# Performance work log

Measured on AMD Instinct MI355X. Metric: run time of the kernel, lower is better.

The kernel has to match this reference:

```python
import jax, jax.numpy as jnp
import numpy as np

B, T, HID = 1, 1024, 2048
H, DK, DV, M, KW = 16, 128, 128, 128, 4  # heads, key dim, value dim, slots, conv kernel
SCALE = DK ** -0.5
EPS = 1e-5


def short_conv(x, w):
    # causal depthwise conv1d + silu; x: [B,T,C], w: [C,K]
    K = w.shape[1]
    xp = jnp.pad(x, ((0, 0), (K - 1, 0), (0, 0)))
    t = x.shape[1]
    y = sum(xp[:, i:i + t] * w[:, i] for i in range(K))
    return jax.nn.silu(y)


def l2norm(x):
    return x * jax.lax.rsqrt(jnp.sum(x * x, axis=-1, keepdims=True) + 1e-6)


def gsa2_scan(q, k, v, w, g, beta):
    # q,k: [B,T,H,DK]  v: [B,T,H,DV]  w,g: [B,T,H,M]  beta: [B,T,H]
    b = q.shape[0]
    tm = lambda x: jnp.moveaxis(x, 1, 0)  # time-major
    Sk0 = jnp.zeros((b, H, DK, M), q.dtype)  # key->slot memory
    Sv0 = jnp.zeros((b, H, M, DV), q.dtype)  # slot->value memory

    def step(carry, xs):
        Sk, Sv = carry
        q_t, k_t, v_t, w_t, g_t, b_t = xs
        gt = jnp.exp(g_t)  # [B,H,M] gate in (0,1) since g = logsigmoid(.)
        bw = b_t[:, :, None] * w_t  # beta-scaled slot write address [B,H,M]
        Sk = Sk * gt[:, :, None, :] + k_t[..., :, None] * bw[:, :, None, :]
        Sv = Sv * gt[..., None] + bw[..., None] * v_t[:, :, None, :]
        s = jnp.einsum('bhd,bhdm->bhm', q_t, Sk) * SCALE
        a = jax.nn.softmax(s, axis=-1)
        o_t = jnp.einsum('bhm,bhmd->bhd', a, Sv)
        return (Sk, Sv), o_t

    (_, _), o = jax.lax.scan(step, (Sk0, Sv0),
                             (tm(q), tm(k), tm(v), tm(w), tm(g), tm(beta)))
    return jnp.moveaxis(o, 0, 1)  # [B,T,H,DV]


def reference(hidden_states, Wq, Wk, Wv, Ww, cq, ck, cv,
              Wf1, Wf2, Wb, Wg1, Wg2, bg2, norm_w, Wo):
    h = hidden_states  # [B,T,HID]
    q = short_conv(h @ Wq, cq)
    k = short_conv(h @ Wk, ck)
    v = short_conv(h @ Wv, cv)
    w = short_conv(h @ Ww, cv)  # source applies v_conv1d to w (faithful)
    g = jax.nn.log_sigmoid((h @ Wf1) @ Wf2)   # [B,T,H*M]
    beta = jax.nn.sigmoid(h @ Wb)             # [B,T,H]
    rs = lambda x, d: x.reshape(x.shape[0], x.shape[1], -1, d)
    q, k = rs(q, DK), rs(k, DK)
    v = rs(v, DV)
    w = l2norm(rs(w, M))
    g = rs(g, M)
    o = gsa2_scan(q, k, v, w, g, beta)        # [B,T,H,DV]
    gate = rs((h @ Wg1) @ Wg2 + bg2, DV)
    # FusedRMSNormGated with sigmoid activation
    o = o * jax.lax.rsqrt(jnp.mean(o * o, axis=-1, keepdims=True) + EPS)
    o = o * norm_w * jax.nn.sigmoid(gate)
    o = o.reshape(o.shape[0], o.shape[1], -1)
    return o @ Wo


def setup_inputs() -> dict:
    key = jax.random.key(0)
    ks = jax.random.split(key, 16)
    s = 0.02
    return {
        'hidden_states': jax.random.normal(ks[0], (B, T, HID), jnp.float32),
        'Wq': jax.random.normal(ks[1], (HID, H * DK), jnp.float32) * s,
        'Wk': jax.random.normal(ks[2], (HID, H * DK), jnp.float32) * s,
        'Wv': jax.random.normal(ks[3], (HID, H * DV), jnp.float32) * s,
        'Ww': jax.random.normal(ks[4], (HID, H * M), jnp.float32) * s,
        'cq': jax.random.normal(ks[5], (H * DK, KW), jnp.float32) * 0.2,
        'ck': jax.random.normal(ks[6], (H * DK, KW), jnp.float32) * 0.2,
        'cv': jax.random.normal(ks[7], (H * DV, KW), jnp.float32) * 0.2,
        'Wf1': jax.random.normal(ks[8], (HID, DV), jnp.float32) * s,
        'Wf2': jax.random.normal(ks[9], (DV, H * M), jnp.float32) * s,
        'Wb': jax.random.normal(ks[10], (HID, H), jnp.float32) * s,
        'Wg1': jax.random.normal(ks[11], (HID, DV), jnp.float32) * s,
        'Wg2': jax.random.normal(ks[12], (DV, H * DV), jnp.float32) * s,
        'bg2': jnp.zeros((H * DV,), jnp.float32),
        'norm_w': jnp.ones((DV,), jnp.float32),
        'Wo': jax.random.normal(ks[13], (H * DV, HID), jnp.float32) * s,
    }
```

## Files before the change

### kernel.cpp

```cpp
#include <hip/hip_runtime.h>
#include <hip/hip_bf16.h>
#include <stdint.h>

typedef unsigned short u16;
typedef __attribute__((ext_vector_type(8))) short bf16x8;
typedef __attribute__((ext_vector_type(4))) short bf16x4;
typedef __attribute__((ext_vector_type(4))) float f32x4;

#define DEV static __device__ __forceinline__

DEV u16 f2bf(float f){
  union { float f; unsigned u; } x; x.f = f;
  unsigned r = x.u + 0x7fffu + ((x.u >> 16) & 1u);
  return (u16)(r >> 16);
}

DEV float bf2f(u16 u){
  union { unsigned u; float f; } x; x.u = ((unsigned)u) << 16; return x.f;
}

DEV bf16x8 ldfrag(const u16* p){
  bf16x4 a = *(const bf16x4*)p;
  bf16x4 b = *(const bf16x4*)(p+4);
  bf16x8 r;
  r[0]=a[0]; r[1]=a[1]; r[2]=a[2]; r[3]=a[3];
  r[4]=b[0]; r[5]=b[1]; r[6]=b[2]; r[7]=b[3];
  return r;
}

DEV bf16x4 cvt4(float a, float b, float c, float d){
  bf16x4 r; r[0]=(short)f2bf(a); r[1]=(short)f2bf(b); r[2]=(short)f2bf(c); r[3]=(short)f2bf(d);
  return r;
}

DEV void g2l16(const void* g, void* l){
  __builtin_amdgcn_global_load_lds((const __attribute__((address_space(1))) unsigned int*)g,
                                   (__attribute__((address_space(3))) unsigned int*)l,
                                   16, 0, 0);
}

__global__ __launch_bounds__(256)
void transp64_k(const float* __restrict__ Wq, const float* __restrict__ Wk,
                const float* __restrict__ Wv, const float* __restrict__ Ww,
                const float* __restrict__ Wo, u16* __restrict__ WcatT, u16* __restrict__ WoT,
                const float* __restrict__ hX, u16* __restrict__ h_bf,
                const float* __restrict__ Wf1, const float* __restrict__ Wg1,
                const float* __restrict__ Wf2, const float* __restrict__ Wg2,
                u16* __restrict__ WfgT, u16* __restrict__ Wf2T, u16* __restrict__ Wg2T){
  __shared__ float tile[64*65];
  const int z = blockIdx.z;
  if (z == 5){
    int idx = ((blockIdx.y*32 + blockIdx.x)*256 + threadIdx.x)*8;
    float4 v0 = *(const float4*)&hX[idx];
    float4 v1 = *(const float4*)&hX[idx+4];
    ushort4 o0, o1;
    o0.x=f2bf(v0.x); o0.y=f2bf(v0.y); o0.z=f2bf(v0.z); o0.w=f2bf(v0.w);
    o1.x=f2bf(v1.x); o1.y=f2bf(v1.y); o1.z=f2bf(v1.z); o1.w=f2bf(v1.w);
    *(ushort4*)&h_bf[idx]   = o0;
    *(ushort4*)&h_bf[idx+4] = o1;
    return;
  }
  if (z >= 6){
    int rem = blockIdx.y*32 + blockIdx.x;
    if (rem >= 256) return;
    const float* src; u16* dst; int R, C, cx, cy;
    if (z==6){      src=Wf1; dst=WfgT;                  R=2048; C=128;  cx=rem&3;  cy=rem>>2; }
    else if (z==7){ src=Wg1; dst=WfgT+(size_t)128*2048; R=2048; C=128;  cx=rem&3;  cy=rem>>2; }
    else if (z==8){ src=Wf2; dst=Wf2T;                  R=128;  C=2048; cx=rem>>2; cy=rem&3; }
    else {          src=Wg2; dst=Wg2T;                  R=128;  C=2048; cx=rem>>2; cy=rem&3; }
    const int c0 = cx*32, r0 = cy*32;
    const int x = threadIdx.x & 31, y0 = threadIdx.x >> 5;
#pragma unroll
    for (int j=0;j<4;j++){
      int r = y0 + j*8;
      tile[r*33 + x] = src[(size_t)(r0+r)*C + c0 + x];
    }
    __syncthreads();
#pragma unroll
    for (int j=0;j<4;j++){
      int cc = y0 + j*8;
      dst[(size_t)(c0+cc)*R + r0 + x] = f2bf(tile[x*33 + cc]);
    }
    return;
  }
  const float* src = (z==0)?Wq:((z==1)?Wk:((z==2)?Wv:((z==3)?Ww:Wo)));
  u16* dst = (z<4) ? (WcatT + (size_t)z*4194304) : WoT;
  const int c0 = blockIdx.x*64, r0 = blockIdx.y*64;
#pragma unroll
  for (int p=0;p<4;p++){
    int i = threadIdx.x + p*256;
    int r = i>>4, c4 = (i&15)<<2;
    *(float4*)&tile[r*65 + c4] = *(const float4*)&src[(size_t)(r0+r)*2048 + c0 + c4];
  }
  __syncthreads();
#pragma unroll
  for (int p=0;p<4;p++){
    int i = threadIdx.x + p*256;
    int cc = i>>4, r4 = (i&15)<<2;
    ushort4 o;
    o.x = f2bf(tile[(r4+0)*65 + cc]); o.y = f2bf(tile[(r4+1)*65 + cc]);
    o.z = f2bf(tile[(r4+2)*65 + cc]); o.w = f2bf(tile[(r4+3)*65 + cc]);
    *(ushort4*)&dst[(size_t)(c0+cc)*2048 + r0 + r4] = o;
  }
}

template<bool OBF>
__global__ __launch_bounds__(256)
void gemm4_k(const u16* __restrict__ A, const u16* __restrict__ B, void* __restrict__ Cp,
             int K, int lda, int ldb, int ldc){
  __shared__ u16 As[2][128*64];
  __shared__ u16 Bs[2][128*64];
  const int m0 = blockIdx.y*128, n0 = blockIdx.x*128;
  const int tid = threadIdx.x;
  const int wave = tid>>6, lane = tid&63, lr = lane&15, kg = lane>>4;
  const int wm = wave>>1, wn = wave&1;
  const f32x4 vz = {0.f,0.f,0.f,0.f};
  f32x4 acc[4][4];
#pragma unroll
  for (int a=0;a<4;a++)
#pragma unroll
    for (int b=0;b<4;b++) acc[a][b]=vz;

#define STAGE4(buf, k0) do { \
    _Pragma("unroll") \
    for (int p=0;p<4;p++){ \
      int chunk = tid + p*256, r_ = chunk>>3, ci = chunk&7; \
      g2l16(A + (size_t)(m0+r_)*lda + (k0) + ((ci^(r_&7))<<3), &As[buf][chunk*8]); \
    } \
    _Pragma("unroll") \
    for (int p=0;p<4;p++){ \
      int chunk = tid + p*256, r_ = chunk>>3, ci = chunk&7; \
      g2l16(B + (size_t)(n0+r_)*ldb + (k0) + ((ci^(r_&7))<<3), &Bs[buf][chunk*8]); \
    } \
  } while(0)

  const int nt = K>>6;
  STAGE4(0, 0);
  STAGE4(1, 64);
  for (int t=0; t<nt; ++t){
    const int buf = t&1;
    if (t < nt-1) asm volatile("s_waitcnt vmcnt(8)" ::: "memory");
    else          asm volatile("s_waitcnt vmcnt(0)" ::: "memory");
    asm volatile("s_barrier" ::: "memory");
#pragma unroll
    for (int ks=0; ks<2; ++ks){
      bf16x8 af[4], bfv[4];
#pragma unroll
      for (int mi=0;mi<4;mi++){
        int r = wm*64+mi*16+lr;
        af[mi] = *(const bf16x8*)&As[buf][r*64 + (((ks*4+kg)^(r&7))<<3)];
      }
#pragma unroll
      for (int ni=0;ni<4;ni++){
        int r = wn*64+ni*16+lr;
        bfv[ni] = *(const bf16x8*)&Bs[buf][r*64 + (((ks*4+kg)^(r&7))<<3)];
      }
      asm volatile("s_waitcnt lgkmcnt(0)" ::: "memory");
      __builtin_amdgcn_sched_barrier(0);
      __builtin_amdgcn_s_setprio(1);
#pragma unroll
      for (int mi=0;mi<4;mi++)
#pragma unroll
        for (int ni=0;ni<4;ni++)
          acc[mi][ni] = __builtin_amdgcn_mfma_f32_16x16x32_bf16(af[mi], bfv[ni], acc[mi][ni], 0, 0, 0);
      __builtin_amdgcn_s_setprio(0);
      __builtin_amdgcn_sched_barrier(0);
      asm volatile("s_barrier" ::: "memory");
    }
    if (t+2 < nt) STAGE4(buf, (t+2)<<6);
  }
#undef STAGE4
#pragma unroll
  for (int mi=0;mi<4;mi++)
#pragma unroll
    for (int ni=0;ni<4;ni++)
#pragma unroll
      for (int vv=0;vv<4;vv++){
        int row = m0 + wm*64 + mi*16 + kg*4 + vv;
        int col = n0 + wn*64 + ni*16 + lr;
        if (OBF) ((u16*)Cp)[(size_t)row*ldc + col] = f2bf(acc[mi][ni][vv]);
        else     ((float*)Cp)[(size_t)row*ldc + col] = acc[mi][ni][vv];
      }
}

__global__ __launch_bounds__(256)
void gemm4sk_k(const u16* __restrict__ A, const u16* __restrict__ B, float* __restrict__ P,
               int Khalf, int lda, int ldb, int ldc){
  __shared__ u16 As[2][128*64];
  __shared__ u16 Bs[2][128*64];
  const int m0 = blockIdx.y*128, n0 = blockIdx.x*128;
  const int kbase = blockIdx.z*Khalf;
  const int tid = threadIdx.x;
  const int wave = tid>>6, lane = tid&63, lr = lane&15, kg = lane>>4;
  const int wm = wave>>1, wn = wave&1;
  const f32x4 vz = {0.f,0.f,0.f,0.f};
  f32x4 acc[4][4];
#pragma unroll
  for (int a=0;a<4;a++)
#pragma unroll
    for (int b=0;b<4;b++) acc[a][b]=vz;

#define STAGE4(buf, k0) do { \
    _Pragma("unroll") \
    for (int p=0;p<4;p++){ \
      int chunk = tid + p*256, r_ = chunk>>3, ci = chunk&7; \
      g2l16(A + (size_t)(m0+r_)*lda + (k0) + ((ci^(r_&7))<<3), &As[buf][chunk*8]); \
    } \
    _Pragma("unroll") \
    for (int p=0;p<4;p++){ \
      int chunk = tid + p*256, r_ = chunk>>3, ci = chunk&7; \
      g2l16(B + (size_t)(n0+r_)*ldb + (k0) + ((ci^(r_&7))<<3), &Bs[buf][chunk*8]); \
    } \
  } while(0)

  const int nt = Khalf>>6;
  STAGE4(0, kbase);
  STAGE4(1, kbase+64);
  for (int t=0; t<nt; ++t){
    const int buf = t&1;
    if (t < nt-1) asm volatile("s_waitcnt vmcnt(8)" ::: "memory");
    else          asm volatile("s_waitcnt vmcnt(0)" ::: "memory");
    asm volatile("s_barrier" ::: "memory");
#pragma unroll
    for (int ks=0; ks<2; ++ks){
      bf16x8 af[4], bfv[4];
#pragma unroll
      for (int mi=0;mi<4;mi++){
        int r = wm*64+mi*16+lr;
        af[mi] = *(const bf16x8*)&As[buf][r*64 + (((ks*4+kg)^(r&7))<<3)];
      }
#pragma unroll
      for (int ni=0;ni<4;ni++){
        int r = wn*64+ni*16+lr;
        bfv[ni] = *(const bf16x8*)&Bs[buf][r*64 + (((ks*4+kg)^(r&7))<<3)];
      }
      asm volatile("s_waitcnt lgkmcnt(0)" ::: "memory");
      __builtin_amdgcn_sched_barrier(0);
      __builtin_amdgcn_s_setprio(1);
#pragma unroll
      for (int mi=0;mi<4;mi++)
#pragma unroll
        for (int ni=0;ni<4;ni++)
          acc[mi][ni] = __builtin_amdgcn_mfma_f32_16x16x32_bf16(af[mi], bfv[ni], acc[mi][ni], 0, 0, 0);
      __builtin_amdgcn_s_setprio(0);
      __builtin_amdgcn_sched_barrier(0);
      asm volatile("s_barrier" ::: "memory");
    }
    if (t+2 < nt) STAGE4(buf, kbase + ((t+2)<<6));
  }
#undef STAGE4
#pragma unroll
  for (int mi=0;mi<4;mi++)
#pragma unroll
    for (int ni=0;ni<4;ni++)
#pragma unroll
      for (int vv=0;vv<4;vv++){
        int row = m0 + wm*64 + mi*16 + kg*4 + vv;
        int col = n0 + wn*64 + ni*16 + lr;
        P[(size_t)blockIdx.z*2097152 + (size_t)row*ldc + col] = acc[mi][ni][vv];
      }
}

__global__ __launch_bounds__(256)
void addout_k(const float* __restrict__ P, float* __restrict__ out){
  int i = (blockIdx.x*256 + threadIdx.x)*4;
  float4 a = *(const float4*)&P[i];
  float4 b = *(const float4*)&P[2097152 + i];
  float4 s = {a.x+b.x, a.y+b.y, a.z+b.z, a.w+b.w};
  *(float4*)&out[i] = s;
}

__global__ __launch_bounds__(256)
void gemmg_k(const u16* __restrict__ f1g1, const u16* __restrict__ Bf, const u16* __restrict__ Bg,
             float* __restrict__ Cf, float* __restrict__ Cg){
  __shared__ u16 As[128*32];
  __shared__ u16 Bs[128*32];
  const int zz = blockIdx.z;
  const u16* A = f1g1 + zz*128;
  const u16* B = zz ? Bg : Bf;
  float* C = zz ? Cg : Cf;
  const int m0 = blockIdx.y*128, n0 = blockIdx.x*128;
  const int tid = threadIdx.x;
  const int lane = tid & 63, wave = tid >> 6;
  const int wr = wave >> 1, wc = wave & 1;
  const int lr = lane & 15, kg = lane >> 4;
  const f32x4 vzero = {0.f,0.f,0.f,0.f};
  f32x4 acc[4][4];
#pragma unroll
  for (int a=0;a<4;a++)
#pragma unroll
    for (int b=0;b<4;b++) acc[a][b] = vzero;
  const int r0 = tid>>2, s0 = tid&3;
  for (int k0=0;k0<128;k0+=32){
    __syncthreads();
    g2l16(A + (size_t)(m0+r0)*256 + k0 + s0*8, (u16*)As + (size_t)tid*8);
    g2l16(B + (size_t)(n0+r0)*128 + k0 + s0*8, (u16*)Bs + (size_t)tid*8);
    g2l16(A + (size_t)(m0+r0+64)*256 + k0 + s0*8, (u16*)As + (size_t)(tid+256)*8);
    g2l16(B + (size_t)(n0+r0+64)*128 + k0 + s0*8, (u16*)Bs + (size_t)(tid+256)*8);
    __syncthreads();
    bf16x8 af[4], bfv[4];
#pragma unroll
    for (int mi=0;mi<4;mi++) af[mi]  = *(const bf16x8*)(As + (wr*64+mi*16+lr)*32 + kg*8);
#pragma unroll
    for (int ni=0;ni<4;ni++) bfv[ni] = *(const bf16x8*)(Bs + (wc*64+ni*16+lr)*32 + kg*8);
#pragma unroll
    for (int mi=0;mi<4;mi++)
#pragma unroll
      for (int ni=0;ni<4;ni++)
        acc[mi][ni] = __builtin_amdgcn_mfma_f32_16x16x32_bf16(af[mi], bfv[ni], acc[mi][ni], 0, 0, 0);
  }
#pragma unroll
  for (int mi=0;mi<4;mi++)
#pragma unroll
    for (int ni=0;ni<4;ni++)
#pragma unroll
      for (int vv=0;vv<4;vv++){
        int row = m0 + wr*64 + mi*16 + kg*4 + vv;
        int col = n0 + wc*64 + ni*16 + lr;
        float val = acc[mi][ni][vv];
        if (zz==0) val = fminf(val,0.f) - __logf(1.f + __expf(-fabsf(val)));
        C[(size_t)row*2048 + col] = val;
      }
}

__global__ __launch_bounds__(256)
void gemmsk_k(const u16* __restrict__ A, const u16* __restrict__ B, float* __restrict__ P,
              int lda, int ldb){
  __shared__ u16 As[128*32];
  __shared__ u16 Bs[128*32];
  const int m0 = blockIdx.y*128, n0 = blockIdx.x*128;
  const int kbase = blockIdx.z*128;
  const int tid = threadIdx.x;
  const int lane = tid & 63, wave = tid >> 6;
  const int wr = wave >> 1, wc = wave & 1;
  const int lr = lane & 15, kg = lane >> 4;
  const f32x4 vzero = {0.f,0.f,0.f,0.f};
  f32x4 acc[4][4];
#pragma unroll
  for (int a=0;a<4;a++)
#pragma unroll
    for (int b=0;b<4;b++) acc[a][b] = vzero;
  const int r0 = tid>>2, s0 = tid&3;
  for (int k0=kbase;k0<kbase+128;k0+=32){
    __syncthreads();
    g2l16(A + (size_t)(m0+r0)*lda + k0 + s0*8, (u16*)As + (size_t)tid*8);
    g2l16(B + (size_t)(n0+r0)*ldb + k0 + s0*8, (u16*)Bs + (size_t)tid*8);
    g2l16(A + (size_t)(m0+r0+64)*lda + k0 + s0*8, (u16*)As + (size_t)(tid+256)*8);
    g2l16(B + (size_t)(n0+r0+64)*ldb + k0 + s0*8, (u16*)Bs + (size_t)(tid+256)*8);
    __syncthreads();
    bf16x8 af[4], bfv[4];
#pragma unroll
    for (int mi=0;mi<4;mi++) af[mi]  = *(const bf16x8*)(As + (wr*64+mi*16+lr)*32 + kg*8);
#pragma unroll
    for (int ni=0;ni<4;ni++) bfv[ni] = *(const bf16x8*)(Bs + (wc*64+ni*16+lr)*32 + kg*8);
#pragma unroll
    for (int mi=0;mi<4;mi++)
#pragma unroll
      for (int ni=0;ni<4;ni++)
        acc[mi][ni] = __builtin_amdgcn_mfma_f32_16x16x32_bf16(af[mi], bfv[ni], acc[mi][ni], 0, 0, 0);
  }
#pragma unroll
  for (int mi=0;mi<4;mi++)
#pragma unroll
    for (int ni=0;ni<4;ni++)
#pragma unroll
      for (int vv=0;vv<4;vv++){
        int row = m0 + wr*64 + mi*16 + kg*4 + vv;
        int col = n0 + wc*64 + ni*16 + lr;
        P[(size_t)blockIdx.z*262144 + (size_t)row*256 + col] = acc[mi][ni][vv];
      }
}

__global__ __launch_bounds__(256)
void reduce16_k(const float* __restrict__ P, u16* __restrict__ out){
  int i = (blockIdx.x*256 + threadIdx.x)*4;
  float4 s = *(const float4*)&P[i];
#pragma unroll
  for (int z=1;z<16;z++){
    float4 p = *(const float4*)&P[(size_t)z*262144 + i];
    s.x+=p.x; s.y+=p.y; s.z+=p.z; s.w+=p.w;
  }
  ushort4 o; o.x=f2bf(s.x); o.y=f2bf(s.y); o.z=f2bf(s.z); o.w=f2bf(s.w);
  *(ushort4*)&out[i] = o;
}

__global__ __launch_bounds__(256)
void beta_k(const float* __restrict__ h, const float* __restrict__ Wb, float* __restrict__ betab){
  __shared__ float hrow[2048];
  __shared__ float red[16][5];
  const int t = blockIdx.x, tid = threadIdx.x;
#pragma unroll
  for (int j=0;j<8;j++) hrow[tid + j*256] = h[(size_t)t*2048 + tid + j*256];
  __syncthreads();
  float part[16];
#pragma unroll
  for (int n=0;n<16;n++) part[n]=0.f;
  for (int j=0;j<8;j++){
    int kk = tid + j*256;
    float hv = hrow[kk];
    const float4* wr4 = (const float4*)&Wb[(size_t)kk*16];
    float4 w0=wr4[0], w1=wr4[1], w2=wr4[2], w3=wr4[3];
    part[0]+=hv*w0.x; part[1]+=hv*w0.y; part[2]+=hv*w0.z; part[3]+=hv*w0.w;
    part[4]+=hv*w1.x; part[5]+=hv*w1.y; part[6]+=hv*w1.z; part[7]+=hv*w1.w;
    part[8]+=hv*w2.x; part[9]+=hv*w2.y; part[10]+=hv*w2.z; part[11]+=hv*w2.w;
    part[12]+=hv*w3.x; part[13]+=hv*w3.y; part[14]+=hv*w3.z; part[15]+=hv*w3.w;
  }
#pragma unroll
  for (int n=0;n<16;n++){
    float s = part[n];
#pragma unroll
    for (int off=1;off<64;off<<=1) s += __shfl_xor(s, off);
    if ((tid&63)==0) red[n][tid>>6] = s;
  }
  __syncthreads();
  if (tid < 16){
    float s = red[tid][0]+red[tid][1]+red[tid][2]+red[tid][3];
    betab[t*16+tid] = 1.f/(1.f+__expf(-s));
  }
}

__global__ __launch_bounds__(256)
void conv_k(const u16* __restrict__ raw, const float* __restrict__ cq,
            const float* __restrict__ ck, const float* __restrict__ cv,
            const float* __restrict__ betab,
            u16* __restrict__ qo, u16* __restrict__ ko,
            u16* __restrict__ vo, float* __restrict__ bwout){
  __shared__ float red[2][2][4];
  int idx = blockIdx.x*256 + threadIdx.x;
  int cgl = idx & 8191, tb = idx >> 13;
  int which = cgl >> 11, cc = cgl & 2047;
  const float* wt = (which==0)?cq:((which==1)?ck:cv);
  float4 w4 = *(const float4*)&wt[cc*4];
  int t0 = tb*4;
  float x[7];
#pragma unroll
  for (int j=0;j<7;j++){
    int t = t0 - 3 + j;
    x[j] = (t >= 0) ? bf2f(raw[(size_t)t*8192 + cgl]) : 0.f;
  }
  float y[4];
#pragma unroll
  for (int j=0;j<4;j++){
    float yy = x[j]*w4.x + x[j+1]*w4.y + x[j+2]*w4.z + x[j+3]*w4.w;
    y[j] = yy / (1.f + __expf(-yy));
  }
  if (which < 3){
    u16* outb = (which==0)?qo:((which==1)?ko:vo);
#pragma unroll
    for (int j=0;j<4;j++)
      outb[(size_t)(t0+j)*2048 + cc] = f2bf(y[j]);
  } else {
    const int hh = threadIdx.x >> 7;
    const int wh = (threadIdx.x >> 6) & 1;
    float ss[4];
#pragma unroll
    for (int j=0;j<4;j++){
      float s = y[j]*y[j];
#pragma unroll
      for (int off=1;off<64;off<<=1) s += __shfl_xor(s, off);
      ss[j] = s;
    }
    if ((threadIdx.x & 63) == 0){
#pragma unroll
      for (int j=0;j<4;j++) red[hh][wh][j] = ss[j];
    }
    __syncthreads();
    const int h = cc >> 7;
#pragma unroll
    for (int j=0;j<4;j++){
      float tot = red[hh][0][j] + red[hh][1][j];
      float r = rsqrtf(tot + 1e-6f) * betab[(t0+j)*16 + h];
      bwout[(size_t)(t0+j)*2048 + cc] = y[j]*r;
    }
  }
}

__global__ __launch_bounds__(128)
void cg_k(const float* __restrict__ gpre, float* __restrict__ cg){
  int idx = blockIdx.x*128 + threadIdx.x;
  int c = idx >> 11;
  size_t base = (size_t)(idx & 2047);
  float run = 0.f;
  for (int i2=0;i2<64;i2++){
    size_t t = (size_t)c*64 + i2;
    run += gpre[t*2048 + base];
    cg[t*2048 + base] = run;
  }
}

__global__ __launch_bounds__(256)
void phaseA_k(const u16* __restrict__ k, const u16* __restrict__ v,
              const float* __restrict__ bw, const float* __restrict__ cg,
              u16* __restrict__ DSkT, u16* __restrict__ DSvT){
  __shared__ u16 UT[128*68];
  __shared__ u16 KT[128*68];
  __shared__ u16 VT[128*68];
  __shared__ float Gt[128];
  const int bx=blockIdx.x, h=bx&15, c=bx>>4, tid=threadIdx.x;
  const int w=tid>>6, lane=tid&63, lr=lane&15, kg=lane>>4;
  if (tid<128) Gt[tid] = cg[(size_t)(c*64+63)*2048 + h*128 + tid];
  __syncthreads();
#pragma unroll
  for (int j=0;j<8;j++){
    int f4=tid+j*256, r=f4>>5, c4=(f4&31)<<2;
    size_t g=(size_t)(c*64+r)*2048 + h*128 + c4;
    ushort4 kv=*(const ushort4*)&k[g];
    ushort4 vv=*(const ushort4*)&v[g];
    float4 bv=*(const float4*)&bw[g];
    float4 cv=*(const float4*)&cg[g];
    float u0=bv.x*__expf(Gt[c4+0]-cv.x);
    float u1=bv.y*__expf(Gt[c4+1]-cv.y);
    float u2=bv.z*__expf(Gt[c4+2]-cv.z);
    float u3=bv.w*__expf(Gt[c4+3]-cv.w);
    KT[(c4+0)*68+r]=kv.x; KT[(c4+1)*68+r]=kv.y;
    KT[(c4+2)*68+r]=kv.z; KT[(c4+3)*68+r]=kv.w;
    VT[(c4+0)*68+r]=vv.x; VT[(c4+1)*68+r]=vv.y;
    VT[(c4+2)*68+r]=vv.z; VT[(c4+3)*68+r]=vv.w;
    UT[(c4+0)*68+r]=f2bf(u0);   UT[(c4+1)*68+r]=f2bf(u1);
    UT[(c4+2)*68+r]=f2bf(u2);   UT[(c4+3)*68+r]=f2bf(u3);
  }
  __syncthreads();
  const f32x4 vz = {0.f,0.f,0.f,0.f};
  {
    f32x4 acc[2][8];
#pragma unroll
    for (int a=0;a<2;a++)
#pragma unroll
      for (int b=0;b<8;b++) acc[a][b]=vz;
#pragma unroll
    for (int ks=0;ks<2;ks++){
      bf16x8 a0=ldfrag(&UT[(w*32   +lr)*68 + ks*32+kg*8]);
      bf16x8 a1=ldfrag(&UT[(w*32+16+lr)*68 + ks*32+kg*8]);
#pragma unroll
      for (int nj=0;nj<8;nj++){
        bf16x8 b=ldfrag(&KT[(nj*16+lr)*68 + ks*32+kg*8]);
        acc[0][nj]=__builtin_amdgcn_mfma_f32_16x16x32_bf16(a0,b,acc[0][nj],0,0,0);
        acc[1][nj]=__builtin_amdgcn_mfma_f32_16x16x32_bf16(a1,b,acc[1][nj],0,0,0);
      }
    }
#pragma unroll
    for (int mi2=0;mi2<2;mi2++)
#pragma unroll
      for (int nj=0;nj<8;nj++)
#pragma unroll
        for (int vv2=0;vv2<4;vv2++)
          DSkT[(size_t)bx*16384 + (size_t)(w*32+mi2*16+kg*4+vv2)*128 + nj*16+lr] = f2bf(acc[mi2][nj][vv2]);
  }
  {
    f32x4 acc[2][8];
#pragma unroll
    for (int a=0;a<2;a++)
#pragma unroll
      for (int b=0;b<8;b++) acc[a][b]=vz;
#pragma unroll
    for (int ks=0;ks<2;ks++){
      bf16x8 a0=ldfrag(&VT[(w*32   +lr)*68 + ks*32+kg*8]);
      bf16x8 a1=ldfrag(&VT[(w*32+16+lr)*68 + ks*32+kg*8]);
#pragma unroll
      for (int nj=0;nj<8;nj++){
        bf16x8 b=ldfrag(&UT[(nj*16+lr)*68 + ks*32+kg*8]);
        acc[0][nj]=__builtin_amdgcn_mfma_f32_16x16x32_bf16(a0,b,acc[0][nj],0,0,0);
        acc[1][nj]=__builtin_amdgcn_mfma_f32_16x16x32_bf16(a1,b,acc[1][nj],0,0,0);
      }
    }
#pragma unroll
    for (int mi2=0;mi2<2;mi2++)
#pragma unroll
      for (int nj=0;nj<8;nj++)
#pragma unroll
        for (int vv2=0;vv2<4;vv2++)
          DSvT[(size_t)bx*16384 + (size_t)(w*32+mi2*16+kg*4+vv2)*128 + nj*16+lr] = f2bf(acc[mi2][nj][vv2]);
  }
}

__global__ __launch_bounds__(256)
void phaseB_k(const u16* __restrict__ DSk, const u16* __restrict__ DSv,
              const float* __restrict__ cg, u16* __restrict__ Sk0, u16* __restrict__ Sv0){
  unsigned idx = blockIdx.x*256u + threadIdx.x;
  int sel  = idx >> 18;
  int h    = (idx >> 14) & 15;
  int flat = idx & 16383;
  int mdec = sel ? (flat & 127) : (flat >> 7);
  const u16* DS = sel ? DSv : DSk;
  u16* S = sel ? Sv0 : Sk0;
  float cur = 0.f;
  for (int c=0;c<16;c++){
    size_t sb = ((size_t)(c*16+h))*16384 + flat;
    S[sb] = f2bf(cur);
    float gd = __expf(cg[(size_t)(c*64+63)*2048 + h*128 + mdec]);
    cur = cur*gd + bf2f(DS[sb]);
  }
}

__global__ __launch_bounds__(256)
void phaseC_k(const u16* __restrict__ q, const u16* __restrict__ k,
              const u16* __restrict__ v, const float* __restrict__ bw,
              const float* __restrict__ cg, const u16* __restrict__ SkT,
              const u16* __restrict__ SvT, float* __restrict__ o){
  __shared__ u16 Qb[64*132];
  __shared__ u16 KV[8704];
  __shared__ u16 Bws[64*132];
  __shared__ u16 BwT[128*68];
  __shared__ u16 Ssb[64*68];
  __shared__ u16 SkL[128*132];
  __shared__ u16 SvL[128*132];
  __shared__ float cgm[128];
  __shared__ float ecgm[128];
  const int bx=blockIdx.x, h=bx&15, c=bx>>4, tid=threadIdx.x;
  const int w=tid>>6, lane=tid&63, lr=lane&15, kg=lane>>4;
  const float SCALE = 0.088388347648318447f;
  const f32x4 vz = {0.f,0.f,0.f,0.f};
  if (tid<128){ float t=cg[(size_t)(c*64+31)*2048 + h*128 + tid]; cgm[tid]=t; ecgm[tid]=__expf(t); }
  __syncthreads();
#pragma unroll
  for (int j=0;j<8;j++){
    int f4=tid+j*256, r=f4>>5, c4=(f4&31)<<2;
    size_t g=(size_t)(c*64+r)*2048 + h*128 + c4;
    *(ushort4*)&Qb[r*132+c4] = *(const ushort4*)&q[g];
    *(ushort4*)&KV[r*132+c4] = *(const ushort4*)&k[g];
    float4 bv=*(const float4*)&bw[g];
    float4 cv=*(const float4*)&cg[g];
    float b0=bv.x*__expf(cgm[c4+0]-cv.x);
    float b1=bv.y*__expf(cgm[c4+1]-cv.y);
    float b2=bv.z*__expf(cgm[c4+2]-cv.z);
    float b3=bv.w*__expf(cgm[c4+3]-cv.w);
    bf16x4 bb = cvt4(b0,b1,b2,b3);
    *(bf16x4*)&Bws[r*132+c4] = bb;
    BwT[(c4+0)*68+r]=(u16)bb[0]; BwT[(c4+1)*68+r]=(u16)bb[1];
    BwT[(c4+2)*68+r]=(u16)bb[2]; BwT[(c4+3)*68+r]=(u16)bb[3];
  }
  __syncthreads();
  {
    f32x4 acc1[4];
#pragma unroll
    for (int a=0;a<4;a++) acc1[a]=vz;
#pragma unroll
    for (int ks=0;ks<4;ks++){
      bf16x8 aq = ldfrag(&Qb[(w*16+lr)*132 + ks*32+kg*8]);
#pragma unroll
      for (int ni=0;ni<4;ni++){
        bf16x8 bk = ldfrag(&KV[(ni*16+lr)*132 + ks*32+kg*8]);
        acc1[ni]=__builtin_amdgcn_mfma_f32_16x16x32_bf16(aq,bk,acc1[ni],0,0,0);
      }
    }
#pragma unroll
    for (int ni=0;ni<4;ni++)
#pragma unroll
      for (int vv2=0;vv2<4;vv2++){
        int row=w*16+kg*4+vv2, col=ni*16+lr;
        Ssb[row*68+col] = (col<=row) ? f2bf(acc1[ni][vv2]) : (u16)0;
      }
  }
  __syncthreads();
#pragma unroll
  for (int j=0;j<8;j++){
    int f4=tid+j*256, r=f4>>5, c4=(f4&31)<<2;
    ushort4 vv=*(const ushort4*)&v[(size_t)(c*64+r)*2048 + h*128 + c4];
    KV[(c4+0)*68+r]=vv.x; KV[(c4+1)*68+r]=vv.y;
    KV[(c4+2)*68+r]=vv.z; KV[(c4+3)*68+r]=vv.w;
  }
#pragma unroll
  for (int j=0;j<16;j++){
    int f4=tid+j*256, r=f4>>5, c4=(f4&31)<<2;
    ushort4 s4=*(const ushort4*)&SkT[(size_t)bx*16384 + (size_t)r*128 + c4];
    float em=ecgm[r];
    *(bf16x4*)&SkL[r*132+c4]=cvt4(bf2f(s4.x)*em, bf2f(s4.y)*em, bf2f(s4.z)*em, bf2f(s4.w)*em);
  }
#pragma unroll
  for (int j=0;j<16;j++){
    int f4=tid+j*256, r=f4>>5, c4=(f4&31)<<2;
    ushort4 s4=*(const ushort4*)&SvT[(size_t)bx*16384 + (size_t)r*128 + c4];
    *(bf16x4*)&SvL[r*132+c4]=cvt4(bf2f(s4.x)*ecgm[c4+0], bf2f(s4.y)*ecgm[c4+1],
                                  bf2f(s4.z)*ecgm[c4+2], bf2f(s4.w)*ecgm[c4+3]);
  }
  f32x4 zac[8];
#pragma unroll
  for (int a=0;a<8;a++) zac[a]=vz;
#pragma unroll
  for (int ks=0;ks<2;ks++){
    bf16x8 as_ = ldfrag(&Ssb[(w*16+lr)*68 + ks*32+kg*8]);
#pragma unroll
    for (int ni=0;ni<8;ni++){
      bf16x8 bb = ldfrag(&BwT[(ni*16+lr)*68 + ks*32+kg*8]);
      zac[ni]=__builtin_amdgcn_mfma_f32_16x16x32_bf16(as_,bb,zac[ni],0,0,0);
    }
  }
  __syncthreads();
#pragma unroll
  for (int dt=0;dt<4;dt++){
    bf16x8 aq = ldfrag(&Qb[(w*16+lr)*132 + dt*32+kg*8]);
#pragma unroll
    for (int ni=0;ni<8;ni++){
      bf16x8 bs = ldfrag(&SkL[(ni*16+lr)*132 + dt*32+kg*8]);
      zac[ni]=__builtin_amdgcn_mfma_f32_16x16x32_bf16(aq,bs,zac[ni],0,0,0);
    }
  }
  float dec[4][8], zz[4][8];
#pragma unroll
  for (int vv2=0;vv2<4;vv2++)
#pragma unroll
    for (int ni=0;ni<8;ni++) zz[vv2][ni]=zac[ni][vv2];
#pragma unroll
  for (int vv2=0;vv2<4;vv2++){
    size_t gr=(size_t)(c*64+w*16+kg*4+vv2)*2048 + h*128;
#pragma unroll
    for (int ni=0;ni<8;ni++){
      float cgv = cg[gr + ni*16+lr];
      dec[vv2][ni] = __expf(cgv - cgm[ni*16+lr]);
    }
  }
#pragma unroll
  for (int vv2=0;vv2<4;vv2++){
    float mx=-3.0e38f;
#pragma unroll
    for (int ni=0;ni<8;ni++){ zz[vv2][ni] *= SCALE*dec[vv2][ni]; mx=fmaxf(mx,zz[vv2][ni]); }
    mx=fmaxf(mx,__shfl_xor(mx,1)); mx=fmaxf(mx,__shfl_xor(mx,2));
    mx=fmaxf(mx,__shfl_xor(mx,4)); mx=fmaxf(mx,__shfl_xor(mx,8));
    float sum=0.f;
#pragma unroll
    for (int ni=0;ni<8;ni++){ zz[vv2][ni]=__expf(zz[vv2][ni]-mx); sum+=zz[vv2][ni]; }
    sum+=__shfl_xor(sum,1); sum+=__shfl_xor(sum,2);
    sum+=__shfl_xor(sum,4); sum+=__shfl_xor(sum,8);
    float inv=1.f/sum;
#pragma unroll
    for (int ni=0;ni<8;ni++) zz[vv2][ni] *= inv*dec[vv2][ni];
  }
#pragma unroll
  for (int vv2=0;vv2<4;vv2++)
#pragma unroll
    for (int ni=0;ni<8;ni++)
      Qb[(w*16+kg*4+vv2)*132 + ni*16+lr] = f2bf(zz[vv2][ni]);
  {
    f32x4 acc4[4];
#pragma unroll
    for (int a=0;a<4;a++) acc4[a]=vz;
#pragma unroll
    for (int ks=0;ks<4;ks++){
      bf16x8 aa = ldfrag(&Qb[(w*16+lr)*132 + ks*32+kg*8]);
#pragma unroll
      for (int ni=0;ni<4;ni++){
        bf16x8 bb = ldfrag(&Bws[(ni*16+lr)*132 + ks*32+kg*8]);
        acc4[ni]=__builtin_amdgcn_mfma_f32_16x16x32_bf16(aa,bb,acc4[ni],0,0,0);
      }
    }
#pragma unroll
    for (int ni=0;ni<4;ni++)
#pragma unroll
      for (int vv2=0;vv2<4;vv2++){
        int row=w*16+kg*4+vv2, col=ni*16+lr;
        Ssb[row*68+col] = (col<=row) ? f2bf(acc4[ni][vv2]) : (u16)0;
      }
  }
  f32x4 oac[8];
#pragma unroll
  for (int a=0;a<8;a++) oac[a]=vz;
#pragma unroll
  for (int ks=0;ks<2;ks++){
    bf16x8 ap = ldfrag(&Ssb[(w*16+lr)*68 + ks*32+kg*8]);
#pragma unroll
    for (int ni=0;ni<8;ni++){
      bf16x8 bv2 = ldfrag(&KV[(ni*16+lr)*68 + ks*32+kg*8]);
      oac[ni]=__builtin_amdgcn_mfma_f32_16x16x32_bf16(ap,bv2,oac[ni],0,0,0);
    }
  }
#pragma unroll
  for (int mt=0;mt<4;mt++){
    bf16x8 aa = ldfrag(&Qb[(w*16+lr)*132 + mt*32+kg*8]);
#pragma unroll
    for (int ni=0;ni<8;ni++){
      bf16x8 bs = ldfrag(&SvL[(ni*16+lr)*132 + mt*32+kg*8]);
      oac[ni]=__builtin_amdgcn_mfma_f32_16x16x32_bf16(aa,bs,oac[ni],0,0,0);
    }
  }
#pragma unroll
  for (int ni=0;ni<8;ni++)
#pragma unroll
    for (int vv2=0;vv2<4;vv2++)
      o[(size_t)(c*64+w*16+kg*4+vv2)*2048 + h*128 + ni*16+lr] = oac[ni][vv2];
}

__global__ __launch_bounds__(256)
void norm_k(const float* __restrict__ o, const float* __restrict__ gate,
            const float* __restrict__ bg2, const float* __restrict__ nw,
            u16* __restrict__ Obf){
  int row = blockIdx.x*4 + (threadIdx.x>>6);
  int lane = threadIdx.x & 63;
  int t = row >> 4, h = row & 15;
  size_t base = (size_t)t*2048 + h*128;
  float o0 = o[base+lane], o1 = o[base+64+lane];
  float ss = o0*o0 + o1*o1;
#pragma unroll
  for (int off=1;off<64;off<<=1) ss += __shfl_xor(ss, off);
  float r = rsqrtf(ss*(1.f/128.f) + 1e-5f);
  int hv0 = h*128+lane, hv1 = hv0+64;
  float g0 = gate[base+lane]    + bg2[hv0];
  float g1 = gate[base+64+lane] + bg2[hv1];
  float v0 = o0*r*nw[lane]   *(1.f/(1.f+__expf(-g0)));
  float v1 = o1*r*nw[lane+64]*(1.f/(1.f+__expf(-g1)));
  Obf[base+lane]    = f2bf(v0);
  Obf[base+64+lane] = f2bf(v1);
}

extern "C" void kernel_launch(void* const* d_in, const int* in_sizes, int n_in,
                              void* d_out, int out_size, void* d_ws, size_t ws_size,
                              hipStream_t stream){
  (void)in_sizes; (void)n_in; (void)out_size; (void)ws_size;
  const float* hX   = (const float*)d_in[0];
  const float* Wq   = (const float*)d_in[1];
  const float* Wk   = (const float*)d_in[2];
  const float* Wv   = (const float*)d_in[3];
  const float* Ww   = (const float*)d_in[4];
  const float* cq   = (const float*)d_in[5];
  const float* ck   = (const float*)d_in[6];
  const float* cv   = (const float*)d_in[7];
  const float* Wf1  = (const float*)d_in[8];
  const float* Wf2  = (const float*)d_in[9];
  const float* Wb   = (const float*)d_in[10];
  const float* Wg1  = (const float*)d_in[11];
  const float* Wg2  = (const float*)d_in[12];
  const float* bg2  = (const float*)d_in[13];
  const float* nw   = (const float*)d_in[14];
  const float* Wo   = (const float*)d_in[15];
  char* ws = (char*)d_ws;
  u16*   h_bf  = (u16*)  (ws + 0);
  u16*   WcatT = (u16*)  (ws + 4194304);
  u16*   Sk0   = (u16*)  (ws + 4194304);
  u16*   Sv0   = (u16*)  (ws + 20971520);
  u16*   WoT   = (u16*)  (ws + 37748736);
  u16*   WfgT  = (u16*)  (ws + 46137344);
  u16*   Wf2T  = (u16*)  (ws + 47185920);
  u16*   Wg2T  = (u16*)  (ws + 47710208);
  u16*   qkvw  = (u16*)  (ws + 48234496);
  u16*   DSk   = (u16*)  (ws + 48234496);
  u16*   DSv   = (u16*)  (ws + 56623104);
  float* Pw    = (float*)(ws + 48234496);
  float* gateb = (float*)(ws + 65011712);
  u16*   qb    = (u16*)  (ws + 81788928);
  u16*   kb    = (u16*)  (ws + 90177536);
  u16*   vb    = (u16*)  (ws + 98566144);
  float* P8    = (float*)(ws + 106954752);
  float* osc   = (float*)(ws + 106954752);
  float* bwb   = (float*)(ws + 115343360);
  u16*   f1g1  = (u16*)  (ws + 123731968);
  float* gpre  = (float*)(ws + 124256256);
  float* cgb   = (float*)(ws + 132644864);
  float* betab = (float*)(ws + 141033472);
  u16*   Obf   = (u16*)  (ws + 141099008);
  float* outp  = (float*)d_out;

  transp64_k<<<dim3(32,32,10),256,0,stream>>>(Wq, Wk, Wv, Ww, Wo, WcatT, WoT, hX, h_bf,
                                              Wf1, Wg1, Wf2, Wg2, WfgT, Wf2T, Wg2T);

  gemm4_k<true><<<dim3(64,8),256,0,stream>>>(h_bf, WcatT, qkvw, 2048, 2048, 2048, 8192);
  gemmsk_k<<<dim3(2,8,16),256,0,stream>>>(h_bf, WfgT, P8, 2048, 2048);
  reduce16_k<<<256,256,0,stream>>>(P8, f1g1);
  gemmg_k<<<dim3(16,8,2),256,0,stream>>>(f1g1, Wf2T, Wg2T, gpre, gateb);
  beta_k<<<1024,256,0,stream>>>(hX, Wb, betab);

  conv_k<<<8192,256,0,stream>>>(qkvw, cq, ck, cv, betab, qb, kb, vb, bwb);
  cg_k<<<256,128,0,stream>>>(gpre, cgb);

  phaseA_k<<<256,256,0,stream>>>(kb, vb, bwb, cgb, DSk, DSv);
  phaseB_k<<<2048,256,0,stream>>>(DSk, DSv, cgb, Sk0, Sv0);
  phaseC_k<<<256,256,0,stream>>>(qb, kb, vb, bwb, cgb, Sk0, Sv0, osc);

  norm_k<<<4096,256,0,stream>>>(osc, gateb, bg2, nw, Obf);
  gemm4sk_k<<<dim3(16,8,2),256,0,stream>>>(Obf, WoT, Pw, 1024, 2048, 2048, 2048);
  addout_k<<<2048,256,0,stream>>>(Pw, outp);
}
```

Measured before the change: 191.8 us.

## Fuse gate cumsum into gemm epilogue and RMSNorm-gating into phaseC

The chunk-local cumulative sum of log-sigmoid gates moves into the gemmg_k epilogue, which uses in-register prefix sums plus wave shuffles across each 64-row tile, so cg_k disappears. The output RMSNorm with sigmoid gating is fused into phaseC_k's epilogue, removing norm_k and the fp32 output round trip. The gate projection is stored as bf16, and beta_k reads the bf16 copy of the hidden states. Together these cut two launches and several fp32 global-memory passes, at the cost of bf16 precision on the gate and on beta's input.

```diff
diff --git a/kernel.cpp b/kernel.cpp
--- a/kernel.cpp
+++ b/kernel.cpp
@@ -272,13 +272,12 @@
 
 __global__ __launch_bounds__(256)
 void gemmg_k(const u16* __restrict__ f1g1, const u16* __restrict__ Bf, const u16* __restrict__ Bg,
-             float* __restrict__ Cf, float* __restrict__ Cg){
+             float* __restrict__ Ccg, u16* __restrict__ Cgate){
   __shared__ u16 As[128*32];
   __shared__ u16 Bs[128*32];
   const int zz = blockIdx.z;
   const u16* A = f1g1 + zz*128;
   const u16* B = zz ? Bg : Bf;
-  float* C = zz ? Cg : Cf;
   const int m0 = blockIdx.y*128, n0 = blockIdx.x*128;
   const int tid = threadIdx.x;
   const int lane = tid & 63, wave = tid >> 6;
@@ -309,18 +308,56 @@
       for (int ni=0;ni<4;ni++)
         acc[mi][ni] = __builtin_amdgcn_mfma_f32_16x16x32_bf16(af[mi], bfv[ni], acc[mi][ni], 0, 0, 0);
   }
-#pragma unroll
-  for (int mi=0;mi<4;mi++)
-#pragma unroll
-    for (int ni=0;ni<4;ni++)
-#pragma unroll
-      for (int vv=0;vv<4;vv++){
-        int row = m0 + wr*64 + mi*16 + kg*4 + vv;
-        int col = n0 + wc*64 + ni*16 + lr;
-        float val = acc[mi][ni][vv];
-        if (zz==0) val = fminf(val,0.f) - __logf(1.f + __expf(-fabsf(val)));
-        C[(size_t)row*2048 + col] = val;
-      }
+  if (zz == 0){
+#pragma unroll
+    for (int ni=0;ni<4;ni++){
+      float p[4][4]; float s[4];
+#pragma unroll
+      for (int mi=0;mi<4;mi++){
+        float run = 0.f;
+#pragma unroll
+        for (int vv=0;vv<4;vv++){
+          float v = acc[mi][ni][vv];
+          v = fminf(v,0.f) - __logf(1.f + __expf(-fabsf(v)));
+          run += v; p[mi][vv] = run;
+        }
+        s[mi] = run;
+      }
+      float M = 0.f; float base[4];
+#pragma unroll
+      for (int mi=0;mi<4;mi++){
+        float a0 = __shfl(s[mi], lr);
+        float a1 = __shfl(s[mi], lr+16);
+        float a2 = __shfl(s[mi], lr+32);
+        float a3 = __shfl(s[mi], lr+48);
+        float before = 0.f;
+        if (kg>0) before += a0;
+        if (kg>1) before += a1;
+        if (kg>2) before += a2;
+        base[mi] = M + before;
+        M += a0+a1+a2+a3;
+      }
+#pragma unroll
+      for (int mi=0;mi<4;mi++)
+#pragma unroll
+        for (int vv=0;vv<4;vv++){
+          int row = m0 + wr*64 + mi*16 + kg*4 + vv;
+          int col = n0 + wc*64 + ni*16 + lr;
+          Ccg[(size_t)row*2048 + col] = base[mi] + p[mi][vv];
+        }
+    }
+  } else {
+#pragma unroll
+    for (int mi=0;mi<4;mi++)
+#pragma unroll
+      for (int ni=0;ni<4;ni++)
+#pragma unroll
+        for (int vv=0;vv<4;vv++){
+          int row = m0 + wr*64 + mi*16 + kg*4 + vv;
+          int col = n0 + wc*64 + ni*16 + lr;
+          Cgate[(size_t)row*2048 + col] = f2bf(acc[mi][ni][vv]);
+        }
+  }
 }
 
 __global__ __launch_bounds__(256)
@@ -385,12 +422,17 @@
 }
 
 __global__ __launch_bounds__(256)
-void beta_k(const float* __restrict__ h, const float* __restrict__ Wb, float* __restrict__ betab){
+void beta_k(const u16* __restrict__ h, const float* __restrict__ Wb, float* __restrict__ betab){
   __shared__ float hrow[2048];
   __shared__ float red[16][5];
   const int t = blockIdx.x, tid = threadIdx.x;
-#pragma unroll
-  for (int j=0;j<8;j++) hrow[tid + j*256] = h[(size_t)t*2048 + tid + j*256];
+  {
+    int b8 = tid*8;
+    ushort4 a = *(const ushort4*)&h[(size_t)t*2048 + b8];
+    ushort4 b = *(const ushort4*)&h[(size_t)t*2048 + b8 + 4];
+    hrow[b8+0]=bf2f(a.x); hrow[b8+1]=bf2f(a.y); hrow[b8+2]=bf2f(a.z); hrow[b8+3]=bf2f(a.w);
+    hrow[b8+4]=bf2f(b.x); hrow[b8+5]=bf2f(b.y); hrow[b8+6]=bf2f(b.z); hrow[b8+7]=bf2f(b.w);
+  }
   __syncthreads();
   float part[16];
 #pragma unroll
@@ -472,19 +514,6 @@
       float r = rsqrtf(tot + 1e-6f) * betab[(t0+j)*16 + h];
       bwout[(size_t)(t0+j)*2048 + cc] = y[j]*r;
     }
-  }
-}
-
-__global__ __launch_bounds__(128)
-void cg_k(const float* __restrict__ gpre, float* __restrict__ cg){
-  int idx = blockIdx.x*128 + threadIdx.x;
-  int c = idx >> 11;
-  size_t base = (size_t)(idx & 2047);
-  float run = 0.f;
-  for (int i2=0;i2<64;i2++){
-    size_t t = (size_t)c*64 + i2;
-    run += gpre[t*2048 + base];
-    cg[t*2048 + base] = run;
   }
 }
 
@@ -596,7 +625,9 @@
 void phaseC_k(const u16* __restrict__ q, const u16* __restrict__ k,
               const u16* __restrict__ v, const float* __restrict__ bw,
               const float* __restrict__ cg, const u16* __restrict__ SkT,
-              const u16* __restrict__ SvT, float* __restrict__ o){
+              const u16* __restrict__ SvT, const u16* __restrict__ gate,
+              const float* __restrict__ bg2, const float* __restrict__ nw,
+              u16* __restrict__ Obf){
   __shared__ u16 Qb[64*132];
   __shared__ u16 KV[8704];
   __shared__ u16 Bws[64*132];
@@ -773,32 +804,23 @@
     }
   }
 #pragma unroll
-  for (int ni=0;ni<8;ni++)
-#pragma unroll
-    for (int vv2=0;vv2<4;vv2++)
-      o[(size_t)(c*64+w*16+kg*4+vv2)*2048 + h*128 + ni*16+lr] = oac[ni][vv2];
-}
-
-__global__ __launch_bounds__(256)
-void norm_k(const float* __restrict__ o, const float* __restrict__ gate,
-            const float* __restrict__ bg2, const float* __restrict__ nw,
-            u16* __restrict__ Obf){
-  int row = blockIdx.x*4 + (threadIdx.x>>6);
-  int lane = threadIdx.x & 63;
-  int t = row >> 4, h = row & 15;
-  size_t base = (size_t)t*2048 + h*128;
-  float o0 = o[base+lane], o1 = o[base+64+lane];
-  float ss = o0*o0 + o1*o1;
-#pragma unroll
-  for (int off=1;off<64;off<<=1) ss += __shfl_xor(ss, off);
-  float r = rsqrtf(ss*(1.f/128.f) + 1e-5f);
-  int hv0 = h*128+lane, hv1 = hv0+64;
-  float g0 = gate[base+lane]    + bg2[hv0];
-  float g1 = gate[base+64+lane] + bg2[hv1];
-  float v0 = o0*r*nw[lane]   *(1.f/(1.f+__expf(-g0)));
-  float v1 = o1*r*nw[lane+64]*(1.f/(1.f+__expf(-g1)));
-  Obf[base+lane]    = f2bf(v0);
-  Obf[base+64+lane] = f2bf(v1);
+  for (int vv2=0;vv2<4;vv2++){
+    float ss = 0.f;
+#pragma unroll
+    for (int ni=0;ni<8;ni++) ss += oac[ni][vv2]*oac[ni][vv2];
+    ss += __shfl_xor(ss,1); ss += __shfl_xor(ss,2);
+    ss += __shfl_xor(ss,4); ss += __shfl_xor(ss,8);
+    float rr = rsqrtf(ss*(1.f/128.f) + 1e-5f);
+    int row = c*64 + w*16 + kg*4 + vv2;
+#pragma unroll
+    for (int ni=0;ni<8;ni++){
+      int colh = ni*16+lr;
+      int col  = h*128 + colh;
+      float g = bf2f(gate[(size_t)row*2048 + col]) + bg2[col];
+      float val = oac[ni][vv2]*rr*nw[colh]*(1.f/(1.f+__expf(-g)));
+      Obf[(size_t)row*2048 + col] = f2bf(val);
+    }
+  }
 }
 
 extern "C" void kernel_launch(void* const* d_in, const int* in_sizes, int n_in,
@@ -834,15 +856,13 @@
   u16*   DSk   = (u16*)  (ws + 48234496);
   u16*   DSv   = (u16*)  (ws + 56623104);
   float* Pw    = (float*)(ws + 48234496);
-  float* gateb = (float*)(ws + 65011712);
+  u16*   gateb = (u16*)  (ws + 65011712);
   u16*   qb    = (u16*)  (ws + 81788928);
   u16*   kb    = (u16*)  (ws + 90177536);
   u16*   vb    = (u16*)  (ws + 98566144);
   float* P8    = (float*)(ws + 106954752);
-  float* osc   = (float*)(ws + 106954752);
   float* bwb   = (float*)(ws + 115343360);
   u16*   f1g1  = (u16*)  (ws + 123731968);
-  float* gpre  = (float*)(ws + 124256256);
   float* cgb   = (float*)(ws + 132644864);
   float* betab = (float*)(ws + 141033472);
   u16*   Obf   = (u16*)  (ws + 141099008);
@@ -854,17 +874,15 @@
   gemm4_k<true><<<dim3(64,8),256,0,stream>>>(h_bf, WcatT, qkvw, 2048, 2048, 2048, 8192);
   gemmsk_k<<<dim3(2,8,16),256,0,stream>>>(h_bf, WfgT, P8, 2048, 2048);
   reduce16_k<<<256,256,0,stream>>>(P8, f1g1);
-  gemmg_k<<<dim3(16,8,2),256,0,stream>>>(f1g1, Wf2T, Wg2T, gpre, gateb);
-  beta_k<<<1024,256,0,stream>>>(hX, Wb, betab);
+  gemmg_k<<<dim3(16,8,2),256,0,stream>>>(f1g1, Wf2T, Wg2T, cgb, gateb);
+  beta_k<<<1024,256,0,stream>>>(h_bf, Wb, betab);
 
   conv_k<<<8192,256,0,stream>>>(qkvw, cq, ck, cv, betab, qb, kb, vb, bwb);
-  cg_k<<<256,128,0,stream>>>(gpre, cgb);
 
   phaseA_k<<<256,256,0,stream>>>(kb, vb, bwb, cgb, DSk, DSv);
   phaseB_k<<<2048,256,0,stream>>>(DSk, DSv, cgb, Sk0, Sv0);
-  phaseC_k<<<256,256,0,stream>>>(qb, kb, vb, bwb, cgb, Sk0, Sv0, osc);
-
-  norm_k<<<4096,256,0,stream>>>(osc, gateb, bg2, nw, Obf);
+  phaseC_k<<<256,256,0,stream>>>(qb, kb, vb, bwb, cgb, Sk0, Sv0, gateb, bg2, nw, Obf);
+
   gemm4sk_k<<<dim3(16,8,2),256,0,stream>>>(Obf, WoT, Pw, 1024, 2048, 2048, 2048);
   addout_k<<<2048,256,0,stream>>>(Pw, outp);
 }
```

New measurement: 180.8 us. 1.06x faster.
